# Performance work log

Hardware: AMD Instinct MI355X
Metric: run time of the kernel (lower is better)

## Reference

```python
import jax, jax.numpy as jnp
import numpy as np

DIM = 1024
HEADS = 16
HEAD_DIM = DIM // HEADS
SCALE = DIM ** (-0.5)  # note: module scales by full dim, not head_dim


def setup_inputs() -> dict:
    key = jax.random.key(0)
    k1, k2, k3, k4 = jax.random.split(key, 4)
    B, N = 4, 2048
    x = jax.random.normal(k1, (B, N, DIM), dtype=jnp.float32)
    # nn.Linear(dim, 3*dim, bias=False): weight [3*dim, dim]
    w_qkv = jax.random.normal(k2, (3 * DIM, DIM), dtype=jnp.float32) * (DIM ** -0.5)
    # nn.Linear(dim, dim) with bias
    w_out = jax.random.normal(k3, (DIM, DIM), dtype=jnp.float32) * (DIM ** -0.5)
    b_out = jax.random.normal(k4, (DIM,), dtype=jnp.float32) * 0.01
    return {"x": x, "w_qkv": w_qkv, "w_out": w_out, "b_out": b_out}


def reference(x, w_qkv, w_out, b_out):
    b, n, _ = x.shape
    qkv = jnp.einsum('bnd,ed->bne', x, w_qkv)  # [b, n, 3*dim]
    # rearrange 'b n (qkv h d) -> qkv b h n d'
    qkv = qkv.reshape(b, n, 3, HEADS, HEAD_DIM)
    q, k, v = (qkv[:, :, i].transpose(0, 2, 1, 3) for i in range(3))  # [b, h, n, d]
    dots = jnp.einsum('bhid,bhjd->bhij', q, k) * SCALE
    attn = jax.nn.softmax(dots, axis=-1)
    out = jnp.einsum('bhij,bhjd->bhid', attn, v)
    out = out.transpose(0, 2, 1, 3).reshape(b, n, HEADS * HEAD_DIM)  # [b, n, dim]
    return jnp.einsum('bnd,ed->bne', out, w_out) + b_out
```

## Files before the change

### kernel.cpp

```cpp
#include <hip/hip_runtime.h>

typedef __bf16 bf16_t;
typedef __bf16 bf16x2 __attribute__((ext_vector_type(2)));
typedef __bf16 bf16x4 __attribute__((ext_vector_type(4)));
typedef __bf16 bf16x8 __attribute__((ext_vector_type(8)));
typedef float floatx4 __attribute__((ext_vector_type(4)));

__device__ __forceinline__ void gll16(const void* g, void* l) {
  __builtin_amdgcn_global_load_lds(
      (const __attribute__((address_space(1))) void*)g,
      (__attribute__((address_space(3))) void*)l, 16, 0, 0);
}

__device__ __forceinline__ bf16x8 cvt8(const float4 a, const float4 b) {
  bf16x8 v;
  v[0] = (bf16_t)a.x; v[1] = (bf16_t)a.y; v[2] = (bf16_t)a.z; v[3] = (bf16_t)a.w;
  v[4] = (bf16_t)b.x; v[5] = (bf16_t)b.y; v[6] = (bf16_t)b.z; v[7] = (bf16_t)b.w;
  return v;
}

__global__ __launch_bounds__(256)
void cvt_f32_bf16(const float* __restrict__ src, bf16_t* __restrict__ dst, int n8)
{
  const int i = blockIdx.x * 256 + threadIdx.x;
  if (i < n8) {
    const float4 a = ((const float4*)src)[2 * i];
    const float4 b = ((const float4*)src)[2 * i + 1];
    *(bf16x8*)(dst + (size_t)i * 8) = cvt8(a, b);
  }
}

template<bool A32, bool W32, bool C32>
__global__ __launch_bounds__(256, 2)
void gemm_bt(const void* __restrict__ Av, const void* __restrict__ Wv,
             const float* __restrict__ bias, void* __restrict__ Cv,
             int M, int Nf, int K, int lda, int qcols, float qscale)
{
  __shared__ __align__(16) bf16_t lA[128 * 32];
  __shared__ __align__(16) bf16_t lB[128 * 32];

  const int tid  = threadIdx.x;
  const int wave = tid >> 6;
  const int lane = tid & 63;
  const int q    = lane >> 4;
  const int ln   = lane & 15;
  const int wm   = wave >> 1, wn = wave & 1;

  const int x     = blockIdx.x & 7;
  const int local = blockIdx.x >> 3;
  const int mt = x * 8 + (local & 7);
  const int nt = local >> 3;
  const int m0 = mt << 7, n0 = nt << 7;

  floatx4 acc[4][4] = {};

  for (int k0 = 0; k0 < K; k0 += 32) {
    if constexpr (A32) {
      const float* Af = (const float*)Av;
#pragma unroll
      for (int sub = 0; sub < 2; ++sub) {
        const int r  = sub * 64 + (tid >> 2);
        const int c8 = tid & 3;
        const float* s = Af + (size_t)(m0 + r) * lda + k0 + c8 * 8;
        const float4 f0 = *(const float4*)s;
        const float4 f1 = *(const float4*)(s + 4);
        *(bf16x8*)(lA + r * 32 + (c8 ^ ((r >> 1) & 3)) * 8) = cvt8(f0, f1);
      }
    } else {
      const bf16_t* Ab = (const bf16_t*)Av;
#pragma unroll
      for (int half = 0; half < 2; ++half) {
        const int rbase = half * 64 + wave * 16;
        const int r  = rbase + (lane >> 2);
        const int gc = (lane & 3) ^ ((r >> 1) & 3);
        gll16(Ab + (size_t)(m0 + r) * lda + k0 + gc * 8, lA + rbase * 32);
      }
    }
    if constexpr (W32) {
      const float* Wf = (const float*)Wv;
#pragma unroll
      for (int sub = 0; sub < 2; ++sub) {
        const int r  = sub * 64 + (tid >> 2);
        const int c8 = tid & 3;
        const float* s = Wf + (size_t)(n0 + r) * K + k0 + c8 * 8;
        const float4 f0 = *(const float4*)s;
        const float4 f1 = *(const float4*)(s + 4);
        *(bf16x8*)(lB + r * 32 + (c8 ^ ((r >> 1) & 3)) * 8) = cvt8(f0, f1);
      }
    } else {
      const bf16_t* Wb = (const bf16_t*)Wv;
#pragma unroll
      for (int half = 0; half < 2; ++half) {
        const int rbase = half * 64 + wave * 16;
        const int r  = rbase + (lane >> 2);
        const int gc = (lane & 3) ^ ((r >> 1) & 3);
        gll16(Wb + (size_t)(n0 + r) * K + k0 + gc * 8, lB + rbase * 32);
      }
    }
    __syncthreads();

    bf16x8 af[4], bfr[4];
#pragma unroll
    for (int i = 0; i < 4; ++i) {
      const int r = wm * 64 + i * 16 + ln;
      af[i] = *(const bf16x8*)(lA + r * 32 + (q ^ ((r >> 1) & 3)) * 8);
    }
#pragma unroll
    for (int j = 0; j < 4; ++j) {
      const int r = wn * 64 + j * 16 + ln;
      bfr[j] = *(const bf16x8*)(lB + r * 32 + (q ^ ((r >> 1) & 3)) * 8);
    }
#pragma unroll
    for (int i = 0; i < 4; ++i)
#pragma unroll
      for (int j = 0; j < 4; ++j)
        acc[i][j] = __builtin_amdgcn_mfma_f32_16x16x32_bf16(af[i], bfr[j], acc[i][j], 0, 0, 0);
    __syncthreads();
  }

#pragma unroll
  for (int j = 0; j < 4; ++j) {
    const int col = n0 + wn * 64 + j * 16 + ln;
    const float bv = bias ? bias[col] : 0.0f;
    const float sc = (col < qcols) ? qscale : 1.0f;
#pragma unroll
    for (int i = 0; i < 4; ++i) {
      const int row = m0 + wm * 64 + i * 16 + q * 4;
#pragma unroll
      for (int r = 0; r < 4; ++r) {
        const float val = acc[i][j][r] * sc + bv;
        if constexpr (C32)
          ((float*)Cv)[(size_t)(row + r) * Nf + col] = val;
        else
          ((bf16_t*)Cv)[(size_t)(row + r) * Nf + col] = (bf16_t)val;
      }
    }
  }
}

__global__ __launch_bounds__(256, 2)
void attn_kernel(bf16_t* __restrict__ qkv)
{
  __shared__ __align__(16) bf16_t lK[2][128 * 64];
  __shared__ __align__(16) bf16_t lVT[64 * 128];
  __shared__ __align__(16) bf16_t lP[128 * 128];

  const int tid  = threadIdx.x;
  const int wave = tid >> 6;
  const int lane = tid & 63;
  const int q  = lane >> 4;
  const int ln = lane & 15;
  const int wm = wave >> 1, wn = wave & 1;

  const int hw = blockIdx.x;
  const int w  = (hw & 7) * 128 + (hw >> 3);
  const int qt = w & 15;
  const int h  = (w >> 4) & 15;
  const int b  = w >> 8;

  bf16_t* Qbase = qkv + (size_t)(b * 2048 + qt * 128) * 3072 + h * 64;
  const bf16_t* Kbase = qkv + (size_t)(b * 2048) * 3072 + 1024 + h * 64;
  const bf16_t* Vbase = qkv + (size_t)(b * 2048) * 3072 + 2048 + h * 64;

#pragma unroll
  for (int t = 0; t < 4; ++t) {
    const int rbase = t * 32 + wave * 8;
    const int r  = rbase + (lane >> 3);
    const int gc = (lane & 7) ^ (r & 7);
    gll16(Qbase + (size_t)r * 3072 + gc * 8, lP + rbase * 64);
    gll16(Kbase + (size_t)r * 3072 + gc * 8, lK[0] + rbase * 64);
  }
  __syncthreads();

  bf16x8 qf[4][2];
#pragma unroll
  for (int i = 0; i < 4; ++i) {
    const int r = wm * 64 + i * 16 + ln;
#pragma unroll
    for (int kt = 0; kt < 2; ++kt) {
      const int c = (kt * 4 + q) ^ (r & 7);
      qf[i][kt] = *(const bf16x8*)(lP + r * 64 + c * 8);
    }
  }

  bf16x8 vcur[2][2], vnxt[2][2];
#pragma unroll
  for (int it = 0; it < 2; ++it) {
    const bf16_t* src = Vbase + (size_t)(2 * lane) * 3072 + (wave + it * 4) * 8;
    vcur[it][0] = *(const bf16x8*)src;
    vcur[it][1] = *(const bf16x8*)(src + 3072);
  }

  floatx4 accO[2][4] = {};
  floatx4 accS[2] = {};

  bf16x8 ones;
#pragma unroll
  for (int j = 0; j < 8; ++j) ones[j] = (bf16_t)1.0f;

  for (int jt = 0; jt < 16; ++jt) {
    const bf16_t* lKc = lK[jt & 1];
    bf16_t*       lKn = lK[(jt & 1) ^ 1];

    __syncthreads();

#pragma unroll
    for (int it = 0; it < 2; ++it) {
      const int c = wave + it * 4;
#pragma unroll
      for (int j = 0; j < 8; ++j) {
        const int d  = c * 8 + j;
        const int ch = (lane >> 2) ^ (d & 7);
        bf16x2 pr;
        pr[0] = vcur[it][0][j];
        pr[1] = vcur[it][1][j];
        *(bf16x2*)(lVT + d * 128 + ch * 8 + ((2 * lane) & 7)) = pr;
      }
    }

    bf16x8 kf[4][2];
#pragma unroll
    for (int n = 0; n < 4; ++n) {
      const int r = wn * 64 + n * 16 + ln;
#pragma unroll
      for (int kt = 0; kt < 2; ++kt) {
        const int c = (kt * 4 + q) ^ (r & 7);
        kf[n][kt] = *(const bf16x8*)(lKc + r * 64 + c * 8);
      }
    }

    if (jt < 15) {
      const int j0n = (jt + 1) * 128;
#pragma unroll
      for (int t = 0; t < 4; ++t) {
        const int rbase = t * 32 + wave * 8;
        const int r  = rbase + (lane >> 3);
        const int gc = (lane & 7) ^ (r & 7);
        gll16(Kbase + (size_t)(j0n + r) * 3072 + gc * 8, lKn + rbase * 64);
      }
#pragma unroll
      for (int it = 0; it < 2; ++it) {
        const bf16_t* src = Vbase + (size_t)(j0n + 2 * lane) * 3072 + (wave + it * 4) * 8;
        vnxt[it][0] = *(const bf16x8*)src;
        vnxt[it][1] = *(const bf16x8*)(src + 3072);
      }
    }

    __builtin_amdgcn_s_setprio(1);
#pragma unroll
    for (int i = 0; i < 4; ++i) {
#pragma unroll
      for (int n = 0; n < 4; ++n) {
        floatx4 st = {0.0f, 0.0f, 0.0f, 0.0f};
        st = __builtin_amdgcn_mfma_f32_16x16x32_bf16(kf[i][0], qf[n][0], st, 0, 0, 0);
        st = __builtin_amdgcn_mfma_f32_16x16x32_bf16(kf[i][1], qf[n][1], st, 0, 0, 0);
        bf16x4 pk;
#pragma unroll
        for (int r = 0; r < 4; ++r)
          pk[r] = (bf16_t)__builtin_amdgcn_exp2f(st[r]);
        const int m    = wm * 64 + n * 16 + ln;
        const int tok0 = wn * 64 + i * 16 + q * 4;
        *(bf16x4*)(lP + m * 128 + (((tok0 >> 3) ^ (m & 7)) << 3) + (tok0 & 7)) = pk;
      }
    }
    __builtin_amdgcn_s_setprio(0);

    __syncthreads();

    __builtin_amdgcn_s_setprio(1);
#pragma unroll
    for (int ks = 0; ks < 4; ++ks) {
      bf16x8 bv[4];
#pragma unroll
      for (int n = 0; n < 4; ++n) {
        const int d  = n * 16 + ln;
        const int cc = (ks * 4 + q) ^ (d & 7);
        bv[n] = *(const bf16x8*)(lVT + d * 128 + cc * 8);
      }
#pragma unroll
      for (int i = 0; i < 2; ++i) {
        const int m = wave * 32 + i * 16 + ln;
        const bf16x8 ap = *(const bf16x8*)(lP + m * 128 + (((ks * 4 + q) ^ (m & 7)) << 3));
#pragma unroll
        for (int n = 0; n < 4; ++n)
          accO[i][n] = __builtin_amdgcn_mfma_f32_16x16x32_bf16(ap, bv[n], accO[i][n], 0, 0, 0);
        accS[i] = __builtin_amdgcn_mfma_f32_16x16x32_bf16(ap, ones, accS[i], 0, 0, 0);
      }
    }
    __builtin_amdgcn_s_setprio(0);

    if (jt < 15) {
#pragma unroll
      for (int it = 0; it < 2; ++it) {
        vcur[it][0] = vnxt[it][0];
        vcur[it][1] = vnxt[it][1];
      }
    }
  }

#pragma unroll
  for (int i = 0; i < 2; ++i) {
#pragma unroll
    for (int r = 0; r < 4; ++r) {
      const int row = wave * 32 + i * 16 + q * 4 + r;
      const float rcp = 1.0f / fmaxf(accS[i][r], 1e-20f);
#pragma unroll
      for (int n = 0; n < 4; ++n) {
        const int col = n * 16 + ln;
        Qbase[(size_t)row * 3072 + col] = (bf16_t)(accO[i][n][r] * rcp);
      }
    }
  }
}

extern "C" void kernel_launch(void* const* d_in, const int* in_sizes, int n_in,
                              void* d_out, int out_size, void* d_ws, size_t ws_size,
                              hipStream_t stream)
{
  const float* x     = (const float*)d_in[0];
  const float* w_qkv = (const float*)d_in[1];
  const float* w_out = (const float*)d_in[2];
  const float* b_out = (const float*)d_in[3];
  float* out = (float*)d_out;

  bf16_t* qkv    = (bf16_t*)d_ws;
  bf16_t* xb     = qkv    + (size_t)8192 * 3072;
  bf16_t* wqkvb  = xb     + (size_t)8192 * 1024;
  bf16_t* woutb  = wqkvb  + (size_t)3072 * 1024;

  const float qs = 0.04508422f;

  cvt_f32_bf16<<<dim3(4096), dim3(256), 0, stream>>>(x,     xb,    8192 * 1024 / 8);
  cvt_f32_bf16<<<dim3(1536), dim3(256), 0, stream>>>(w_qkv, wqkvb, 3072 * 1024 / 8);
  cvt_f32_bf16<<<dim3(512),  dim3(256), 0, stream>>>(w_out, woutb, 1024 * 1024 / 8);

  gemm_bt<false, false, false><<<dim3(64 * 24), dim3(256), 0, stream>>>(
      xb, wqkvb, nullptr, qkv, 8192, 3072, 1024, 1024, 1024, qs);
  attn_kernel<<<dim3(1024), dim3(256), 0, stream>>>(qkv);
  gemm_bt<false, false, true><<<dim3(64 * 8), dim3(256), 0, stream>>>(
      qkv, woutb, b_out, out, 8192, 1024, 1024, 3072, 0, 1.0f);
}
```

Baseline: 276.2 us.

## Fuse bf16 conversion kernels and deepen GEMM K-tile to 64

Merges the three fp32-to-bf16 conversion launches into one kernel that picks its source by block index, removing two launches. The GEMM drops its unused fp32 input paths, doubles the LDS K-tile from 32 to 64 with a new 8-way XOR swizzle, and issues two MFMAs per fragment pair per iteration. This halves the barrier count and loop overhead per GEMM. It raises LDS use to 32KB per block and the launch-bounds occupancy hint to 3, which may cost registers.

```diff
diff --git a/kernel.cpp b/kernel.cpp
--- a/kernel.cpp
+++ b/kernel.cpp
@@ -20,24 +20,30 @@
 }
 
 __global__ __launch_bounds__(256)
-void cvt_f32_bf16(const float* __restrict__ src, bf16_t* __restrict__ dst, int n8)
+void cvt_all(const float* __restrict__ x,  bf16_t* __restrict__ xb,
+             const float* __restrict__ wq, bf16_t* __restrict__ wqb,
+             const float* __restrict__ wo, bf16_t* __restrict__ wob)
 {
-  const int i = blockIdx.x * 256 + threadIdx.x;
-  if (i < n8) {
-    const float4 a = ((const float4*)src)[2 * i];
-    const float4 b = ((const float4*)src)[2 * i + 1];
-    *(bf16x8*)(dst + (size_t)i * 8) = cvt8(a, b);
-  }
-}
-
-template<bool A32, bool W32, bool C32>
-__global__ __launch_bounds__(256, 2)
-void gemm_bt(const void* __restrict__ Av, const void* __restrict__ Wv,
+  const int bid = blockIdx.x;
+  const float* s;
+  bf16_t* d;
+  int i;
+  if (bid < 4096)      { s = x;  d = xb;  i = bid * 256 + threadIdx.x; }
+  else if (bid < 5632) { s = wq; d = wqb; i = (bid - 4096) * 256 + threadIdx.x; }
+  else                 { s = wo; d = wob; i = (bid - 5632) * 256 + threadIdx.x; }
+  const float4 a = ((const float4*)s)[2 * i];
+  const float4 b = ((const float4*)s)[2 * i + 1];
+  *(bf16x8*)(d + (size_t)i * 8) = cvt8(a, b);
+}
+
+template<bool C32>
+__global__ __launch_bounds__(256, 3)
+void gemm_bt(const bf16_t* __restrict__ Ab, const bf16_t* __restrict__ Wb,
              const float* __restrict__ bias, void* __restrict__ Cv,
              int M, int Nf, int K, int lda, int qcols, float qscale)
 {
-  __shared__ __align__(16) bf16_t lA[128 * 32];
-  __shared__ __align__(16) bf16_t lB[128 * 32];
+  __shared__ __align__(16) bf16_t lA[128 * 64];
+  __shared__ __align__(16) bf16_t lB[128 * 64];
 
   const int tid  = threadIdx.x;
   const int wave = tid >> 6;
@@ -54,67 +60,43 @@
 
   floatx4 acc[4][4] = {};
 
-  for (int k0 = 0; k0 < K; k0 += 32) {
-    if constexpr (A32) {
-      const float* Af = (const float*)Av;
-#pragma unroll
-      for (int sub = 0; sub < 2; ++sub) {
-        const int r  = sub * 64 + (tid >> 2);
-        const int c8 = tid & 3;
-        const float* s = Af + (size_t)(m0 + r) * lda + k0 + c8 * 8;
-        const float4 f0 = *(const float4*)s;
-        const float4 f1 = *(const float4*)(s + 4);
-        *(bf16x8*)(lA + r * 32 + (c8 ^ ((r >> 1) & 3)) * 8) = cvt8(f0, f1);
-      }
-    } else {
-      const bf16_t* Ab = (const bf16_t*)Av;
-#pragma unroll
-      for (int half = 0; half < 2; ++half) {
-        const int rbase = half * 64 + wave * 16;
-        const int r  = rbase + (lane >> 2);
-        const int gc = (lane & 3) ^ ((r >> 1) & 3);
-        gll16(Ab + (size_t)(m0 + r) * lda + k0 + gc * 8, lA + rbase * 32);
-      }
-    }
-    if constexpr (W32) {
-      const float* Wf = (const float*)Wv;
-#pragma unroll
-      for (int sub = 0; sub < 2; ++sub) {
-        const int r  = sub * 64 + (tid >> 2);
-        const int c8 = tid & 3;
-        const float* s = Wf + (size_t)(n0 + r) * K + k0 + c8 * 8;
-        const float4 f0 = *(const float4*)s;
-        const float4 f1 = *(const float4*)(s + 4);
-        *(bf16x8*)(lB + r * 32 + (c8 ^ ((r >> 1) & 3)) * 8) = cvt8(f0, f1);
-      }
-    } else {
-      const bf16_t* Wb = (const bf16_t*)Wv;
-#pragma unroll
-      for (int half = 0; half < 2; ++half) {
-        const int rbase = half * 64 + wave * 16;
-        const int r  = rbase + (lane >> 2);
-        const int gc = (lane & 3) ^ ((r >> 1) & 3);
-        gll16(Wb + (size_t)(n0 + r) * K + k0 + gc * 8, lB + rbase * 32);
-      }
+  for (int k0 = 0; k0 < K; k0 += 64) {
+#pragma unroll
+    for (int t = 0; t < 4; ++t) {
+      const int rbase = t * 32 + wave * 8;
+      const int r  = rbase + (lane >> 3);
+      const int gc = (lane & 7) ^ (r & 7);
+      gll16(Ab + (size_t)(m0 + r) * lda + k0 + gc * 8, lA + rbase * 64);
+      gll16(Wb + (size_t)(n0 + r) * K   + k0 + gc * 8, lB + rbase * 64);
     }
     __syncthreads();
 
-    bf16x8 af[4], bfr[4];
+    bf16x8 af[4][2], bfr[4][2];
 #pragma unroll
     for (int i = 0; i < 4; ++i) {
       const int r = wm * 64 + i * 16 + ln;
-      af[i] = *(const bf16x8*)(lA + r * 32 + (q ^ ((r >> 1) & 3)) * 8);
+#pragma unroll
+      for (int kt = 0; kt < 2; ++kt) {
+        const int c = (kt * 4 + q) ^ (r & 7);
+        af[i][kt] = *(const bf16x8*)(lA + r * 64 + c * 8);
+      }
     }
 #pragma unroll
     for (int j = 0; j < 4; ++j) {
       const int r = wn * 64 + j * 16 + ln;
-      bfr[j] = *(const bf16x8*)(lB + r * 32 + (q ^ ((r >> 1) & 3)) * 8);
+#pragma unroll
+      for (int kt = 0; kt < 2; ++kt) {
+        const int c = (kt * 4 + q) ^ (r & 7);
+        bfr[j][kt] = *(const bf16x8*)(lB + r * 64 + c * 8);
+      }
     }
 #pragma unroll
     for (int i = 0; i < 4; ++i)
 #pragma unroll
       for (int j = 0; j < 4; ++j)
-        acc[i][j] = __builtin_amdgcn_mfma_f32_16x16x32_bf16(af[i], bfr[j], acc[i][j], 0, 0, 0);
+#pragma unroll
+        for (int kt = 0; kt < 2; ++kt)
+          acc[i][j] = __builtin_amdgcn_mfma_f32_16x16x32_bf16(af[i][kt], bfr[j][kt], acc[i][j], 0, 0, 0);
     __syncthreads();
   }
 
@@ -330,13 +312,11 @@
 
   const float qs = 0.04508422f;
 
-  cvt_f32_bf16<<<dim3(4096), dim3(256), 0, stream>>>(x,     xb,    8192 * 1024 / 8);
-  cvt_f32_bf16<<<dim3(1536), dim3(256), 0, stream>>>(w_qkv, wqkvb, 3072 * 1024 / 8);
-  cvt_f32_bf16<<<dim3(512),  dim3(256), 0, stream>>>(w_out, woutb, 1024 * 1024 / 8);
-
-  gemm_bt<false, false, false><<<dim3(64 * 24), dim3(256), 0, stream>>>(
+  cvt_all<<<dim3(6144), dim3(256), 0, stream>>>(x, xb, w_qkv, wqkvb, w_out, woutb);
+
+  gemm_bt<false><<<dim3(64 * 24), dim3(256), 0, stream>>>(
       xb, wqkvb, nullptr, qkv, 8192, 3072, 1024, 1024, 1024, qs);
   attn_kernel<<<dim3(1024), dim3(256), 0, stream>>>(qkv);
-  gemm_bt<false, false, true><<<dim3(64 * 8), dim3(256), 0, stream>>>(
+  gemm_bt<true><<<dim3(64 * 8), dim3(256), 0, stream>>>(
       qkv, woutb, b_out, out, 8192, 1024, 1024, 3072, 0, 1.0f);
 }
```

Result: faster. 268.9 us (-2.6%).
